# Optimization experiments

Hardware: AMD Instinct MI355X
Metric: run time of the kernel (lower is better)

The kernel has to match this reference:

```python
import jax, jax.numpy as jnp
import numpy as np
import math


def pos_enc_3d(h, w, d, c):
    # Faithful PositionalEncoding3D: channels = ceil(c/6)*2 (made even), sin/cos per axis.
    cpe = int(np.ceil(c / 6) * 2)
    if cpe % 2:
        cpe += 1
    inv_freq = 1.0 / (10000.0 ** (np.arange(0, cpe, 2, dtype=np.float32) / cpe))

    def axis_emb(n):
        s = np.arange(n, dtype=np.float32)[:, None] * inv_freq  # (n, cpe//2)
        return np.concatenate([np.sin(s), np.cos(s)], axis=-1)  # (n, cpe)

    ex = np.broadcast_to(axis_emb(h)[:, None, None, :], (h, w, d, cpe))
    ey = np.broadcast_to(axis_emb(w)[None, :, None, :], (h, w, d, cpe))
    ez = np.broadcast_to(axis_emb(d)[None, None, :, :], (h, w, d, cpe))
    emb = np.concatenate([ex, ey, ez], axis=-1)[..., :c]  # (h,w,d,c)
    return jnp.asarray(np.transpose(emb, (3, 0, 1, 2)))  # (c,h,w,d)


def conv3d(x, w, b):
    # x: (b,c,h,w,d), w: (o,i,3,3,3), padding=1
    y = jax.lax.conv_general_dilated(
        x, w, window_strides=(1, 1, 1), padding=[(1, 1)] * 3,
        dimension_numbers=('NCHWD', 'OIHWD', 'NCHWD'))
    return y + b[None, :, None, None, None]


def setup_inputs() -> dict:
    key = jax.random.key(0)
    ks = jax.random.split(key, 12)
    B, C, H, W, D = 2, 64, 16, 16, 16
    C8 = C // 8
    s_emb = 1.0 / math.sqrt(C)
    s_conv = 1.0 / math.sqrt(C * 27)
    return {
        'x': jax.random.normal(ks[0], (B, C, H, W, D), dtype=jnp.float32),
        'Wq': jax.random.normal(ks[1], (C, C), dtype=jnp.float32) * s_emb,
        'Wk': jax.random.normal(ks[2], (C, C), dtype=jnp.float32) * s_emb,
        'Wv': jax.random.normal(ks[3], (C, C), dtype=jnp.float32) * s_emb,
        'qw': jax.random.normal(ks[4], (C8, C, 3, 3, 3), dtype=jnp.float32) * s_conv,
        'qb': jax.random.normal(ks[5], (C8,), dtype=jnp.float32) * 0.01,
        'kw': jax.random.normal(ks[6], (C8, C, 3, 3, 3), dtype=jnp.float32) * s_conv,
        'kb': jax.random.normal(ks[7], (C8,), dtype=jnp.float32) * 0.01,
        'vw': jax.random.normal(ks[8], (C, C, 3, 3, 3), dtype=jnp.float32) * s_conv,
        'vb': jax.random.normal(ks[9], (C,), dtype=jnp.float32) * 0.01,
        'lam1': jax.random.normal(ks[10], (1,), dtype=jnp.float32) * 0.5,
        'lam2': jax.random.normal(ks[11], (1,), dtype=jnp.float32) * 0.5,
    }


def reference(x, Wq, Wk, Wv, qw, qb, kw, kb, vw, vb, lam1, lam2):
    b, c, h, w, d = x.shape
    n = h * w * d
    # NOTE: torch code does `x += pe` in-place inside SelfAttention, so the
    # PE-added x is also what GSA and the residual see.
    pe = pos_enc_3d(h, w, d, c)  # (c,h,w,d)
    x_pe = x + pe[None]

    # ---- SelfAttention (TSA) ----
    tok = x_pe.reshape(b, c, n).transpose(0, 2, 1)  # (b,n,c)
    Q = jnp.einsum('bnc,cd->bnd', tok, Wq)
    K = jnp.einsum('bnc,cd->bnd', tok, Wk)
    V = jnp.einsum('bnc,cd->bnd', tok, Wv)
    A = jax.nn.softmax(jnp.einsum('bic,bjc->bij', Q, K) / math.sqrt(c), axis=-1)
    tsa = jnp.einsum('bij,bjc->bic', A, V).transpose(0, 2, 1).reshape(b, c, h, w, d)

    # ---- GlobalSpatialAttention (GSA) ----
    M = conv3d(x_pe, qw, qb).reshape(b, c // 8, n)   # (b,c/8,n)
    Nk = conv3d(x_pe, kw, kb).reshape(b, c // 8, n)  # (b,c/8,n)
    Wv_ = conv3d(x_pe, vw, vb).reshape(b, c, n)      # (b,c,n)
    Bm = jax.nn.softmax(jnp.einsum('bci,bcj->bij', M, Nk), axis=-1)  # (b,n,n)
    gsa = jnp.einsum('bcj,bij->bci', Wv_, Bm).reshape(b, c, h, w, d)

    return lam1[0] * tsa + lam2[0] * gsa + x_pe
```

## Files before the change

kernel.cpp:

```cpp
#include <hip/hip_runtime.h>
#include <math.h>

#define BB 2
#define CC 64
#define NN 4096
#define CN (CC*NN)
#define NJ 4
#define NT ((NN/NJ)/64)

#define LOG2E 1.4426950408889634f
#define QSCALE 0.18033688011112042f

#define XT_ROWS 4097
#define WQKV_OFF (27*80*64)

typedef __attribute__((ext_vector_type(8))) short short8;
typedef __attribute__((ext_vector_type(4))) float float4v;
typedef unsigned short ushortT;

__device__ __forceinline__ ushortT f2bf(float x) {
    union { float f; unsigned u; } v; v.f = x;
    unsigned r = v.u + 0x7FFF + ((v.u >> 16) & 1);
    return (ushortT)(r >> 16);
}
__device__ __forceinline__ float bf2f(short s) {
    union { unsigned u; float f; } v;
    v.u = ((unsigned)(unsigned short)s) << 16;
    return v.f;
}
__device__ __forceinline__ unsigned pk2(float a, float b) {
    unsigned ua = __float_as_uint(a) + 0x8000u;
    unsigned ub = __float_as_uint(b) + 0x8000u;
    return __builtin_amdgcn_perm(ub, ua, 0x07060302);
}

__device__ __forceinline__ float pe_tab_val(int c, int pos) {
    int c2 = (c < 22) ? c : (c < 44) ? (c - 22) : (c - 44);
    int is_cos = (c2 >= 11);
    int k = c2 - (is_cos ? 11 : 0);
    float freq = exp2f(-1.2079738526863135f * (float)k);
    float arg = (float)pos * freq;
    return is_cos ? cosf(arg) : sinf(arg);
}

__global__ __launch_bounds__(256) void k_pre(const float* __restrict__ x,
                                             const float* __restrict__ qw,
                                             const float* __restrict__ kw,
                                             const float* __restrict__ vw,
                                             const float* __restrict__ Wq,
                                             const float* __restrict__ Wk,
                                             const float* __restrict__ Wv,
                                             float* __restrict__ xpe,
                                             ushortT* __restrict__ Xt,
                                             ushortT* __restrict__ Wr) {
    int blk = blockIdx.x, t = threadIdx.x;
    if (blk < 256) {
        __shared__ float sPE[64][17];
        __shared__ float sT[64][33];
        int b = blk >> 7, pos0 = (blk & 127) * 32;
        #pragma unroll
        for (int k = 0; k < 4; k++) {
            int e = t + k * 256;
            int c = e >> 4, coord = e & 15;
            sPE[c][coord] = pe_tab_val(c, coord);
        }
        __syncthreads();
        int pin = t & 31, cg = t >> 5;
        #pragma unroll
        for (int pass = 0; pass < 8; pass++) {
            int c = pass * 8 + cg;
            int pos = pos0 + pin;
            int coord = (c < 22) ? (pos >> 8) : (c < 44) ? ((pos >> 4) & 15) : (pos & 15);
            size_t gi = (size_t)(b * 64 + c) * NN + pos;
            float v = x[gi] + sPE[c][coord];
            xpe[gi] = v;
            sT[c][pin] = v;
        }
        __syncthreads();
        int icn = t & 63, pg = t >> 6;
        #pragma unroll
        for (int pass = 0; pass < 8; pass++) {
            int po = pass * 4 + pg;
            Xt[((size_t)b * XT_ROWS + pos0 + po + 1) * 64 + icn] = f2bf(sT[icn][po]);
        }
        if ((blk & 127) == 0 && t < 64)
            Xt[((size_t)b * XT_ROWS) * 64 + t] = 0;
    } else {
        int idx = (blk - 256) * 256 + t;
        if (idx < WQKV_OFF) {
            int ic = idx & 63;
            int oc = (idx >> 6) % 80;
            int tap = idx / 5120;
            float v;
            if (oc < 8)       v = qw[(oc * 64 + ic) * 27 + tap] * LOG2E;
            else if (oc < 16) v = kw[((oc - 8) * 64 + ic) * 27 + tap];
            else              v = vw[((oc - 16) * 64 + ic) * 27 + tap];
            Wr[idx] = f2bf(v);
        } else if (idx < WQKV_OFF + 3 * 64 * 64) {
            int idx2 = idx - WQKV_OFF;
            int c = idx2 & 63, d = (idx2 >> 6) & 63, mat = idx2 >> 12;
            const float* Wm = (mat == 0) ? Wq : (mat == 1) ? Wk : Wv;
            float v = Wm[c * 64 + d] * ((mat == 0) ? QSCALE : 1.f);
            Wr[idx] = f2bf(v);
        }
    }
}

__global__ __launch_bounds__(256) void k_qkv(const ushortT* __restrict__ Xt,
                                             const ushortT* __restrict__ Wr,
                                             ushortT* __restrict__ Qb,
                                             ushortT* __restrict__ Kb,
                                             ushortT* __restrict__ Vtb) {
    __shared__ ushortT sVt[64][72];
    int t = threadIdx.x, w = t >> 6, l = t & 63;
    int lane15 = l & 15, q = l >> 4;
    int mat = blockIdx.y, b = blockIdx.z;
    int i0 = blockIdx.x * 64 + w * 16;

    const ushortT* Wt = Wr + WQKV_OFF + mat * 4096;
    const ushortT* xrow = Xt + ((size_t)b * XT_ROWS + i0 + lane15 + 1) * 64;
    short8 a0 = *(const short8*)(xrow + q * 8);
    short8 a1 = *(const short8*)(xrow + 32 + q * 8);
    float4v acc[4];
    #pragma unroll
    for (int cg = 0; cg < 4; cg++) {
        const ushortT* wrow = Wt + (cg * 16 + lane15) * 64;
        short8 b0 = *(const short8*)(wrow + q * 8);
        short8 b1 = *(const short8*)(wrow + 32 + q * 8);
        float4v a = (float4v)0.f;
        a = __builtin_amdgcn_mfma_f32_16x16x32_bf16(a0, b0, a, 0, 0, 0);
        a = __builtin_amdgcn_mfma_f32_16x16x32_bf16(a1, b1, a, 0, 0, 0);
        acc[cg] = a;
    }
    if (mat < 2) {
        ushortT* o = (mat == 0) ? Qb : Kb;
        #pragma unroll
        for (int cg = 0; cg < 4; cg++)
            #pragma unroll
            for (int r = 0; r < 4; r++)
                o[((size_t)(b * NN + i0 + q * 4 + r)) * 64 + cg * 16 + lane15] = f2bf(acc[cg][r]);
    } else {
        int il = w * 16 + q * 4;
        #pragma unroll
        for (int cg = 0; cg < 4; cg++)
            #pragma unroll
            for (int r = 0; r < 4; r++)
                sVt[cg * 16 + lane15][il + r] = f2bf(acc[cg][r]);
        __syncthreads();
        int c2 = t >> 2, seg = t & 3;
        short8 v0 = *(const short8*)&sVt[c2][seg * 16];
        short8 v1 = *(const short8*)&sVt[c2][seg * 16 + 8];
        size_t base = ((size_t)(b * 64 + c2)) * NN + blockIdx.x * 64 + seg * 16;
        *(short8*)(Vtb + base) = v0;
        *(short8*)(Vtb + base + 8) = v1;
    }
}

template<int IS_TSA>
__device__ __forceinline__ void stage_load(short8* kst, short8* vst,
                                           const ushortT* __restrict__ Km,
                                           const ushortT* __restrict__ Vt,
                                           int b, int jb, int t) {
    if (IS_TSA) {
        #pragma unroll
        for (int ps = 0; ps < 2; ps++) {
            int idx = ps * 256 + t, j = idx >> 3, g = idx & 7;
            kst[ps] = *(const short8*)(Km + ((size_t)(b * NN + jb + j)) * 64 + g * 8);
        }
    } else {
        if (t < 64)
            kst[0] = *(const short8*)(Km + ((size_t)(b * NN + jb + t)) * 8);
    }
    #pragma unroll
    for (int ps = 0; ps < 2; ps++) {
        int idx = ps * 256 + t, c = idx >> 3, gj = idx & 7;
        vst[ps] = *(const short8*)(Vt + ((size_t)(b * 64 + c)) * NN + jb + gj * 8);
    }
}

template<int IS_TSA>
__device__ __forceinline__ void stage_write(const short8* kst, const short8* vst,
                                            ushortT* sK, ushortT* sV, int t) {
    if (IS_TSA) {
        #pragma unroll
        for (int ps = 0; ps < 2; ps++) {
            int idx = ps * 256 + t, j = idx >> 3, g = idx & 7;
            *(short8*)(sK + j * 64 + ((g ^ (j & 7)) * 8)) = kst[ps];
        }
    } else {
        if (t < 64)
            *(short8*)(sK + t * 64 + ((t & 7) * 8)) = kst[0];
    }
    #pragma unroll
    for (int ps = 0; ps < 2; ps++) {
        int idx = ps * 256 + t, c = idx >> 3, gj = idx & 7;
        *(short8*)(sV + c * 64 + ((gj ^ (c & 7)) * 8)) = vst[ps];
    }
}

template<int IS_TSA>
__device__ __forceinline__ void flash_body(int it, int jc, int b, int t,
                                           const ushortT* __restrict__ Qm,
                                           const ushortT* __restrict__ Km,
                                           const ushortT* __restrict__ Vt,
                                           float* __restrict__ pM,
                                           float* __restrict__ pL,
                                           ushortT* __restrict__ pAcc,
                                           ushortT* __restrict__ sKb,
                                           ushortT* __restrict__ sVb,
                                           ushortT* __restrict__ sPall) {
    constexpr int KCH = IS_TSA ? 2 : 1;
    constexpr int DQ  = IS_TSA ? 64 : 8;
    int w = t >> 6, l = t & 63;
    int lane15 = l & 15, q = l >> 4;
    int i0 = it * 64 + w * 16;
    ushortT* myP = sPall + w * (16 * 64);

    short8 qf[KCH];
    {
        const ushortT* qrow = Qm + ((size_t)(b * NN + i0 + lane15)) * DQ;
        if (IS_TSA) {
            qf[0] = *(const short8*)(qrow + q * 8);
            qf[1] = *(const short8*)(qrow + 32 + q * 8);
        } else {
            short8 z = (short8)0;
            if (q == 0) z = *(const short8*)qrow;
            qf[0] = z;
        }
    }

    float m_run = -3e38f, Lacc = 0.f;
    float4v O[4];
    #pragma unroll
    for (int cs = 0; cs < 4; cs++) O[cs] = (float4v)0.f;

    const int jbase0 = jc * (NN / NJ);

    short8 kst[2], vst[2];
    stage_load<IS_TSA>(kst, vst, Km, Vt, b, jbase0, t);
    stage_write<IS_TSA>(kst, vst, sKb, sVb, t);
    __syncthreads();

    for (int jt = 0; jt < NT; jt++) {
        int cur = jt & 1;
        ushortT* cK = sKb + cur * 4096;
        ushortT* cV = sVb + cur * 4096;
        bool more = (jt + 1 < NT);

        if (more) stage_load<IS_TSA>(kst, vst, Km, Vt, b, jbase0 + (jt + 1) * 64, t);

        short8 kf[4][KCH];
        #pragma unroll
        for (int sub = 0; sub < 4; sub++) {
            int jr = sub * 16 + lane15;
            if (IS_TSA) {
                kf[sub][0] = *(const short8*)(cK + jr * 64 + (((0 * 4 + q) ^ (lane15 & 7)) * 8));
                kf[sub][1] = *(const short8*)(cK + jr * 64 + (((1 * 4 + q) ^ (lane15 & 7)) * 8));
            } else {
                short8 z = (short8)0;
                if (q == 0) z = *(const short8*)(cK + jr * 64 + ((lane15 & 7) * 8));
                kf[sub][0] = z;
            }
        }

        float4v s[4];
        #pragma unroll
        for (int sub = 0; sub < 4; sub++) {
            float4v acc = (float4v)0.f;
            #pragma unroll
            for (int kc = 0; kc < KCH; kc++)
                acc = __builtin_amdgcn_mfma_f32_16x16x32_bf16(kf[sub][kc], qf[kc], acc, 0, 0, 0);
            s[sub] = acc;
        }

        short8 va[4], vbf[4];
        #pragma unroll
        for (int sub = 0; sub < 4; sub++) {
            int cr = sub * 16 + lane15;
            va[sub]  = *(const short8*)(cV + cr * 64 + ((q ^ (lane15 & 7)) * 8));
            vbf[sub] = *(const short8*)(cV + cr * 64 + (((4 + q) ^ (lane15 & 7)) * 8));
        }

        float tmax = fmaxf(fmaxf(fmaxf(s[0][0], s[0][1]), fmaxf(s[0][2], s[0][3])),
                           fmaxf(fmaxf(s[1][0], s[1][1]), fmaxf(s[1][2], s[1][3])));
        float tmax2 = fmaxf(fmaxf(fmaxf(s[2][0], s[2][1]), fmaxf(s[2][2], s[2][3])),
                            fmaxf(fmaxf(s[3][0], s[3][1]), fmaxf(s[3][2], s[3][3])));
        tmax = fmaxf(tmax, tmax2);
        tmax = fmaxf(tmax, __shfl_xor(tmax, 16));
        tmax = fmaxf(tmax, __shfl_xor(tmax, 32));
        float mnew = fmaxf(m_run, tmax);

        if (__any(mnew > m_run)) {
            float corr = exp2f(m_run - mnew);
            Lacc *= corr;
            float c0 = __shfl(corr, q * 4 + 0);
            float c1 = __shfl(corr, q * 4 + 1);
            float c2 = __shfl(corr, q * 4 + 2);
            float c3 = __shfl(corr, q * 4 + 3);
            #pragma unroll
            for (int cs = 0; cs < 4; cs++) {
                O[cs][0] *= c0; O[cs][1] *= c1; O[cs][2] *= c2; O[cs][3] *= c3;
            }
        }
        m_run = mnew;

        #pragma unroll
        for (int sub = 0; sub < 4; sub++) {
            float p0 = exp2f(s[sub][0] - mnew);
            float p1 = exp2f(s[sub][1] - mnew);
            float p2 = exp2f(s[sub][2] - mnew);
            float p3 = exp2f(s[sub][3] - mnew);
            Lacc += (p0 + p1) + (p2 + p3);
            unsigned lo = pk2(p0, p1), hi = pk2(p2, p3);
            int g = sub * 2 + (q >> 1);
            unsigned* wp = (unsigned*)(myP + lane15 * 64 + ((g ^ (lane15 & 7)) * 8) + (q & 1) * 4);
            wp[0] = lo; wp[1] = hi;
        }

        short8 pf0 = *(const short8*)(myP + lane15 * 64 + (((0 * 4 + q) ^ (lane15 & 7)) * 8));
        short8 pf1 = *(const short8*)(myP + lane15 * 64 + (((1 * 4 + q) ^ (lane15 & 7)) * 8));

        #pragma unroll
        for (int sub = 0; sub < 4; sub++) {
            O[sub] = __builtin_amdgcn_mfma_f32_16x16x32_bf16(pf0, va[sub], O[sub], 0, 0, 0);
            O[sub] = __builtin_amdgcn_mfma_f32_16x16x32_bf16(pf1, vbf[sub], O[sub], 0, 0, 0);
        }

        if (more)
            stage_write<IS_TSA>(kst, vst, sKb + (cur ^ 1) * 4096, sVb + (cur ^ 1) * 4096, t);
        __syncthreads();
    }

    size_t base = (size_t)(b * NJ + jc) * NN + i0;
    Lacc += __shfl_xor(Lacc, 16);
    Lacc += __shfl_xor(Lacc, 32);
    if (q == 0) {
        pL[base + lane15] = Lacc;
        pM[base + lane15] = m_run;
    }
    #pragma unroll
    for (int cs = 0; cs < 4; cs++)
        #pragma unroll
        for (int r = 0; r < 4; r++)
            pAcc[(base + q * 4 + r) * 64 + cs * 16 + lane15] = f2bf(O[cs][r]);
}

__global__ __launch_bounds__(256, 4) void k_tsacv(const ushortT* __restrict__ Qb,
                                                  const ushortT* __restrict__ Kb,
                                                  const ushortT* __restrict__ Vtb,
                                                  const ushortT* __restrict__ Xt,
                                                  const ushortT* __restrict__ Wr,
                                                  const float* __restrict__ qb,
                                                  const float* __restrict__ kb,
                                                  const float* __restrict__ vb,
                                                  ushortT* __restrict__ Mt,
                                                  ushortT* __restrict__ Nt,
                                                  ushortT* __restrict__ Wvt,
                                                  float* __restrict__ pMt, float* __restrict__ pLt,
                                                  ushortT* __restrict__ pAccT) {
    __shared__ ushortT sK[2][64 * 64];
    __shared__ ushortT sV[2][64 * 64];
    __shared__ ushortT sP[4][16 * 64];
    int bx = blockIdx.x, t = threadIdx.x;
    if (bx < 512) {
        int it = bx & 63, jc = (bx >> 6) & 3, b = bx >> 8;
        flash_body<1>(it, jc, b, t, Qb, Kb, Vtb, pMt, pLt, pAccT,
                      &sK[0][0], &sV[0][0], &sP[0][0]);
    } else {
        int cv = bx - 512;
        int tile = cv & 63, rest = cv >> 6;
        int ocg = rest % 5, b = rest / 5;
        int w = t >> 6, l = t & 63, lane15 = l & 15, q = l >> 4;
        int pos0 = tile * 64 + w * 16;
        const ushortT* xb = Xt + (size_t)b * XT_ROWS * 64;
        int pos = pos0 + lane15;
        int dz = pos & 15, wy = (pos >> 4) & 15, hx = pos >> 8;
        float4v acc0 = (float4v)0.f, acc1 = (float4v)0.f;
        #pragma unroll
        for (int tap = 0; tap < 27; tap++) {
            const int dh = tap / 9 - 1, dw = (tap / 3) % 3 - 1, dd = tap % 3 - 1;
            const int shift = dh * 256 + dw * 16 + dd;
            const ushortT* wrow = Wr + ((size_t)tap * 80 + ocg * 16 + lane15) * 64 + q * 8;
            short8 a0 = *(const short8*)(wrow);
            short8 a1 = *(const short8*)(wrow + 32);
            bool ok = ((unsigned)(hx + dh) < 16u) &&
                      ((unsigned)(wy + dw) < 16u) &&
                      ((unsigned)(dz + dd) < 16u);
            int row = ok ? (pos + shift + 1) : 0;
            const ushortT* xrow = xb + (size_t)row * 64 + q * 8;
            short8 b0 = *(const short8*)xrow;
            short8 b1 = *(const short8*)(xrow + 32);
            acc0 = __builtin_amdgcn_mfma_f32_16x16x32_bf16(a0, b0, acc0, 0, 0, 0);
            acc1 = __builtin_amdgcn_mfma_f32_16x16x32_bf16(a1, b1, acc1, 0, 0, 0);
        }
        float4v accT = acc0 + acc1;
        if (ocg == 0) {
            #pragma unroll
            for (int r = 0; r < 4; r++) {
                int ol = q * 4 + r;
                float v = accT[r];
                if (ol < 8)
                    Mt[((size_t)(b * NN + pos)) * 8 + ol] = f2bf(v + qb[ol] * LOG2E);
                else
                    Nt[((size_t)(b * NN + pos)) * 8 + (ol - 8)] = f2bf(v + kb[ol - 8]);
            }
        } else {
            #pragma unroll
            for (int r = 0; r < 4; r++) {
                int oc = (ocg - 1) * 16 + q * 4 + r;
                Wvt[((size_t)(b * 64 + oc)) * NN + pos] = f2bf(accT[r] + vb[oc]);
            }
        }
    }
}

__global__ __launch_bounds__(256, 4) void k_gsa(const ushortT* __restrict__ Mtb,
                                                const ushortT* __restrict__ Ntb,
                                                const ushortT* __restrict__ Wvtb,
                                                float* __restrict__ pMg, float* __restrict__ pLg,
                                                ushortT* __restrict__ pAccG) {
    __shared__ ushortT sK[2][64 * 64];
    __shared__ ushortT sV[2][64 * 64];
    __shared__ ushortT sP[4][16 * 64];
    int t = threadIdx.x;
    flash_body<0>(blockIdx.x, blockIdx.y, blockIdx.z, t, Mtb, Ntb, Wvtb, pMg, pLg, pAccG,
                  &sK[0][0], &sV[0][0], &sP[0][0]);
}

__device__ __forceinline__ void reduce_set(const float* __restrict__ pM,
                                           const float* __restrict__ pL,
                                           const ushortT* __restrict__ pAcc,
                                           int b, int n, int seg, float* v) {
    float mv[NJ], M = -3e38f;
    #pragma unroll
    for (int jcc = 0; jcc < NJ; jcc++) {
        mv[jcc] = pM[(size_t)(b * NJ + jcc) * NN + n];
        M = fmaxf(M, mv[jcc]);
    }
    float L = 0.f;
    #pragma unroll
    for (int e = 0; e < 8; e++) v[e] = 0.f;
    #pragma unroll
    for (int jcc = 0; jcc < NJ; jcc++) {
        size_t rb = (size_t)(b * NJ + jcc) * NN + n;
        float wgt = exp2f(mv[jcc] - M);
        L += pL[rb] * wgt;
        short8 x0 = *(const short8*)(pAcc + rb * 64 + seg * 8);
        #pragma unroll
        for (int e = 0; e < 8; e++) v[e] += wgt * bf2f(x0[e]);
    }
    float invL = 1.f / L;
    #pragma unroll
    for (int e = 0; e < 8; e++) v[e] *= invL;
}

__global__ __launch_bounds__(256) void k_reduce(const float* __restrict__ pMt,
                                                const float* __restrict__ pLt,
                                                const ushortT* __restrict__ pAccT,
                                                const float* __restrict__ pMg,
                                                const float* __restrict__ pLg,
                                                const ushortT* __restrict__ pAccG,
                                                const float* __restrict__ xpe,
                                                const float* __restrict__ lam1,
                                                const float* __restrict__ lam2,
                                                float* __restrict__ out) {
    __shared__ float sT[32][65];
    __shared__ float sG[32][65];
    int t = threadIdx.x;
    int b = blockIdx.y;
    int n0 = blockIdx.x * 32;
    int pp = t >> 3, seg = t & 7;
    int n = n0 + pp;

    float vt[8], vg[8];
    reduce_set(pMt, pLt, pAccT, b, n, seg, vt);
    reduce_set(pMg, pLg, pAccG, b, n, seg, vg);
    #pragma unroll
    for (int e = 0; e < 8; e++) {
        sT[pp][seg * 8 + e] = vt[e];
        sG[pp][seg * 8 + e] = vg[e];
    }
    __syncthreads();

    int c = t >> 2, ns = (t & 3) * 8;
    float la1 = lam1[0], la2 = lam2[0];
    size_t ob = ((size_t)(b * 64 + c)) * NN + n0 + ns;
    const float* xp = xpe + ob;
    #pragma unroll
    for (int j = 0; j < 8; j += 4) {
        float4 ov;
        ov.x = la1 * sT[ns + j + 0][c] + la2 * sG[ns + j + 0][c] + xp[j + 0];
        ov.y = la1 * sT[ns + j + 1][c] + la2 * sG[ns + j + 1][c] + xp[j + 1];
        ov.z = la1 * sT[ns + j + 2][c] + la2 * sG[ns + j + 2][c] + xp[j + 2];
        ov.w = la1 * sT[ns + j + 3][c] + la2 * sG[ns + j + 3][c] + xp[j + 3];
        *(float4*)(out + ob + j) = ov;
    }
}

extern "C" void kernel_launch(void* const* d_in, const int* in_sizes, int n_in,
                              void* d_out, int out_size, void* d_ws, size_t ws_size,
                              hipStream_t stream) {
    const float* x    = (const float*)d_in[0];
    const float* Wq   = (const float*)d_in[1];
    const float* Wk   = (const float*)d_in[2];
    const float* Wv   = (const float*)d_in[3];
    const float* qw   = (const float*)d_in[4];
    const float* qb   = (const float*)d_in[5];
    const float* kw   = (const float*)d_in[6];
    const float* kb   = (const float*)d_in[7];
    const float* vw   = (const float*)d_in[8];
    const float* vb   = (const float*)d_in[9];
    const float* lam1 = (const float*)d_in[10];
    const float* lam2 = (const float*)d_in[11];
    float* out = (float*)d_out;

    char* W = (char*)d_ws;
    float*   xpe   = (float*)(W);
    ushortT* Qb    = (ushortT*)(W + (2u << 20));
    ushortT* Kb    = (ushortT*)(W + (3u << 20));
    ushortT* Vtb   = (ushortT*)(W + (4u << 20));
    ushortT* Mtb   = (ushortT*)(W + (5u << 20));
    ushortT* Ntb   = (ushortT*)(W + (5u << 20) + (1u << 17));
    ushortT* Wvtb  = (ushortT*)(W + (5u << 20) + (2u << 17));
    ushortT* Xt    = (ushortT*)(W + (6u << 20) + (2u << 17));
    ushortT* Wr    = (ushortT*)(W + (7u << 20) + (1u << 19));
    float*   pLt   = (float*)(W + (8u << 20));
    float*   pLg   = (float*)(W + (8u << 20) + (1u << 17));
    float*   pMt   = (float*)(W + (8u << 20) + (2u << 17));
    float*   pMg   = (float*)(W + (8u << 20) + (3u << 17));
    ushortT* pAccT = (ushortT*)(W + (8u << 20) + (4u << 17));
    ushortT* pAccG = (ushortT*)(W + (12u << 20) + (4u << 17));

    k_pre<<<dim3(256 + (WQKV_OFF + 3 * 64 * 64 + 255) / 256), dim3(256), 0, stream>>>(
        x, qw, kw, vw, Wq, Wk, Wv, xpe, Xt, Wr);
    k_qkv<<<dim3(64, 3, BB), dim3(256), 0, stream>>>(Xt, Wr, Qb, Kb, Vtb);
    k_tsacv<<<dim3(512 + 640), dim3(256), 0, stream>>>(
        Qb, Kb, Vtb, Xt, Wr, qb, kb, vb, Mtb, Ntb, Wvtb, pMt, pLt, pAccT);
    k_gsa<<<dim3(64, NJ, BB), dim3(256), 0, stream>>>(
        Mtb, Ntb, Wvtb, pMg, pLg, pAccG);
    k_reduce<<<dim3(NN / 32, BB), dim3(256), 0, stream>>>(
        pMt, pLt, pAccT, pMg, pLg, pAccG, xpe, lam1, lam2, out);
}
```

Baseline: 153.2 us.

## Merge conv output-channel groups per block and stage weights in double-buffered LDS

```diff
diff --git a/kernel.cpp b/kernel.cpp
--- a/kernel.cpp
+++ b/kernel.cpp
@@ -358,31 +358,60 @@
                                                   ushortT* __restrict__ Wvt,
                                                   float* __restrict__ pMt, float* __restrict__ pLt,
                                                   ushortT* __restrict__ pAccT) {
-    __shared__ ushortT sK[2][64 * 64];
-    __shared__ ushortT sV[2][64 * 64];
-    __shared__ ushortT sP[4][16 * 64];
+    __shared__ ushortT sm[20480];
     int bx = blockIdx.x, t = threadIdx.x;
     if (bx < 512) {
         int it = bx & 63, jc = (bx >> 6) & 3, b = bx >> 8;
         flash_body<1>(it, jc, b, t, Qb, Kb, Vtb, pMt, pLt, pAccT,
-                      &sK[0][0], &sV[0][0], &sP[0][0]);
+                      sm, sm + 8192, sm + 16384);
     } else {
         int cv = bx - 512;
-        int tile = cv & 63, rest = cv >> 6;
-        int ocg = rest % 5, b = rest / 5;
+        int tile = cv & 63, b = cv >> 6;
         int w = t >> 6, l = t & 63, lane15 = l & 15, q = l >> 4;
         int pos0 = tile * 64 + w * 16;
         const ushortT* xb = Xt + (size_t)b * XT_ROWS * 64;
         int pos = pos0 + lane15;
         int dz = pos & 15, wy = (pos >> 4) & 15, hx = pos >> 8;
-        float4v acc0 = (float4v)0.f, acc1 = (float4v)0.f;
+
+        ushortT* sW = sm;
+
+        float4v accA[5], accB[5];
+        #pragma unroll
+        for (int o = 0; o < 5; o++) { accA[o] = (float4v)0.f; accB[o] = (float4v)0.f; }
+
+        short8 ws[3];
+        auto ldW = [&](int tap) {
+            #pragma unroll
+            for (int c3 = 0; c3 < 3; c3++) {
+                int idx = t + c3 * 256;
+                if (idx < 640)
+                    ws[c3] = *(const short8*)(Wr + (size_t)tap * 5120 + idx * 8);
+            }
+        };
+        auto wrW = [&](ushortT* buf) {
+            #pragma unroll
+            for (int c3 = 0; c3 < 3; c3++) {
+                int idx = t + c3 * 256;
+                if (idx < 640) {
+                    int row = idx >> 3, g = idx & 7;
+                    *(short8*)(buf + row * 64 + ((g ^ (row & 7)) * 8)) = ws[c3];
+                }
+            }
+        };
+
+        ldW(0);
+        wrW(sW);
+        __syncthreads();
+
         #pragma unroll
         for (int tap = 0; tap < 27; tap++) {
             const int dh = tap / 9 - 1, dw = (tap / 3) % 3 - 1, dd = tap % 3 - 1;
             const int shift = dh * 256 + dw * 16 + dd;
-            const ushortT* wrow = Wr + ((size_t)tap * 80 + ocg * 16 + lane15) * 64 + q * 8;
-            short8 a0 = *(const short8*)(wrow);
-            short8 a1 = *(const short8*)(wrow + 32);
+            ushortT* cW = sW + (tap & 1) * 5120;
+            bool more = (tap + 1 < 27);
+
+            if (more) ldW(tap + 1);
+
             bool ok = ((unsigned)(hx + dh) < 16u) &&
                       ((unsigned)(wy + dw) < 16u) &&
                       ((unsigned)(dz + dd) < 16u);
@@ -390,25 +419,39 @@
             const ushortT* xrow = xb + (size_t)row * 64 + q * 8;
             short8 b0 = *(const short8*)xrow;
             short8 b1 = *(const short8*)(xrow + 32);
-            acc0 = __builtin_amdgcn_mfma_f32_16x16x32_bf16(a0, b0, acc0, 0, 0, 0);
-            acc1 = __builtin_amdgcn_mfma_f32_16x16x32_bf16(a1, b1, acc1, 0, 0, 0);
-        }
-        float4v accT = acc0 + acc1;
-        if (ocg == 0) {
-            #pragma unroll
-            for (int r = 0; r < 4; r++) {
-                int ol = q * 4 + r;
-                float v = accT[r];
-                if (ol < 8)
-                    Mt[((size_t)(b * NN + pos)) * 8 + ol] = f2bf(v + qb[ol] * LOG2E);
-                else
-                    Nt[((size_t)(b * NN + pos)) * 8 + (ol - 8)] = f2bf(v + kb[ol - 8]);
+
+            #pragma unroll
+            for (int o = 0; o < 5; o++) {
+                int wr2 = o * 16 + lane15;
+                short8 a0 = *(const short8*)(cW + wr2 * 64 + ((q ^ (lane15 & 7)) * 8));
+                short8 a1 = *(const short8*)(cW + wr2 * 64 + (((4 + q) ^ (lane15 & 7)) * 8));
+                accA[o] = __builtin_amdgcn_mfma_f32_16x16x32_bf16(a0, b0, accA[o], 0, 0, 0);
+                accB[o] = __builtin_amdgcn_mfma_f32_16x16x32_bf16(a1, b1, accB[o], 0, 0, 0);
             }
-        } else {
-            #pragma unroll
-            for (int r = 0; r < 4; r++) {
-                int oc = (ocg - 1) * 16 + q * 4 + r;
-                Wvt[((size_t)(b * 64 + oc)) * NN + pos] = f2bf(accT[r] + vb[oc]);
+
+            if (more) wrW(sW + ((tap + 1) & 1) * 5120);
+            __syncthreads();
+        }
+
+        #pragma unroll
+        for (int o = 0; o < 5; o++) {
+            float4v accT = accA[o] + accB[o];
+            if (o == 0) {
+                #pragma unroll
+                for (int r = 0; r < 4; r++) {
+                    int ol = q * 4 + r;
+                    float v = accT[r];
+                    if (ol < 8)
+                        Mt[((size_t)(b * NN + pos)) * 8 + ol] = f2bf(v + qb[ol] * LOG2E);
+                    else
+                        Nt[((size_t)(b * NN + pos)) * 8 + (ol - 8)] = f2bf(v + kb[ol - 8]);
+                }
+            } else {
+                #pragma unroll
+                for (int r = 0; r < 4; r++) {
+                    int oc = (o - 1) * 16 + q * 4 + r;
+                    Wvt[((size_t)(b * 64 + oc)) * NN + pos] = f2bf(accT[r] + vb[oc]);
+                }
             }
         }
     }
@@ -534,7 +577,7 @@
     k_pre<<<dim3(256 + (WQKV_OFF + 3 * 64 * 64 + 255) / 256), dim3(256), 0, stream>>>(
         x, qw, kw, vw, Wq, Wk, Wv, xpe, Xt, Wr);
     k_qkv<<<dim3(64, 3, BB), dim3(256), 0, stream>>>(Xt, Wr, Qb, Kb, Vtb);
-    k_tsacv<<<dim3(512 + 640), dim3(256), 0, stream>>>(
+    k_tsacv<<<dim3(512 + 128), dim3(256), 0, stream>>>(
         Qb, Kb, Vtb, Xt, Wr, qb, kb, vb, Mtb, Ntb, Wvtb, pMt, pLt, pAccT);
     k_gsa<<<dim3(64, NJ, BB), dim3(256), 0, stream>>>(
         Mtb, Ntb, Wvtb, pMg, pLg, pAccG);
```

Measured after the change: 137.8 us. 1.11x faster.
